# Performance work log

Measured on AMD Instinct MI355X. Metric: run time of the kernel, lower is better.

The kernel has to match this reference:

```python
import jax, jax.numpy as jnp
import numpy as np
from jax import lax

DN = ('NCHW', 'OIHW', 'NCHW')

def conv2d_s2(x, w, b):
    # nn.Conv2d(3,3,kernel=5,stride=2), VALID padding
    y = lax.conv_general_dilated(x, w, (2, 2), 'VALID', dimension_numbers=DN)
    return y + b[None, :, None, None]

def conv_transpose2d_s2_p2(x, w):
    # torch.conv_transpose2d(weight (in,out,5,5), stride=2, padding=2):
    # equivalent to conv with lhs_dilation=2, spatially flipped, IO-transposed kernel,
    # and per-side padding = k-1-p = 2.  Output H -> 2H-2.
    k = jnp.flip(w, (2, 3)).transpose(1, 0, 2, 3)
    return lax.conv_general_dilated(x, k, (1, 1), [(2, 2), (2, 2)],
                                    lhs_dilation=(2, 2), dimension_numbers=DN)

def interp_nearest(x, size):
    # F.interpolate default mode='nearest': src = floor(dst * in/out)
    H, W = x.shape[-2], x.shape[-1]
    oh, ow = size
    ri = (jnp.arange(oh) * H // oh).astype(jnp.int32)
    ci = (jnp.arange(ow) * W // ow).astype(jnp.int32)
    return x[..., ri[:, None], ci[None, :]]

def long_conv(x, conv_w, conv_b, keys, values):
    key = jax.nn.sigmoid(conv2d_s2(x, conv_w, conv_b))      # [1,3,h,w]
    key = interp_nearest(key, (32, 32)).reshape(-1)          # [3072]
    att = jax.nn.softmax(keys @ key)                         # [size]
    kernel = (values * att[:, None]).sum(0).reshape(3, 3, 5, 5)
    return conv_transpose2d_s2_p2(x, kernel)

def looper(x, conv_w, conv_b, keys, values):
    key = jax.nn.sigmoid(conv2d_s2(x, conv_w, conv_b))
    key = interp_nearest(key, (32, 32)).reshape(-1)
    att = jax.nn.softmax(keys @ key)
    return (values * att[:, None]).sum(0)                    # [1]

def setup_inputs() -> dict:
    key = jax.random.key(0)
    ks = jax.random.split(key, 8)
    cw_scale = 1.0 / np.sqrt(3 * 5 * 5)
    return {
        'input': jax.random.uniform(ks[0], (1, 3, 1024, 1024), jnp.float32),
        'lk1_conv_w': jax.random.normal(ks[1], (3, 3, 5, 5), jnp.float32) * cw_scale,
        'lk1_conv_b': jax.random.normal(ks[2], (3,), jnp.float32) * cw_scale,
        'lk1_keys': jax.random.normal(ks[3], (100, 3072), jnp.float32),
        'lk1_values': jax.random.normal(ks[4], (100, 225), jnp.float32),
        'lc_conv_w': jax.random.normal(ks[5], (3, 3, 5, 5), jnp.float32) * cw_scale,
        'lc_conv_b': jax.random.normal(ks[6], (3,), jnp.float32) * cw_scale,
        'lc_keys': jax.random.normal(ks[7], (100, 3072), jnp.float32),
        # values all 3.0 -> Looper output == 3 exactly (softmax sums to 1),
        # sigmoid(3)~0.9526 -> exactly one loop iteration, deterministically.
        'lc_values': jnp.full((100, 1), 3.0, jnp.float32),
    }

def reference(input, lk1_conv_w, lk1_conv_b, lk1_keys, lk1_values,
              lc_conv_w, lc_conv_b, lc_keys, lc_values):
    x = 2.0 * input - 1.0
    out = long_conv(x, lk1_conv_w, lk1_conv_b, lk1_keys, lk1_values)
    ix = float(jax.nn.sigmoid(looper(out, lc_conv_w, lc_conv_b, lc_keys, lc_values))[0])
    it = 0
    # data-dependent loop; exit condition evaluated eagerly (as in the torch code,
    # which syncs to host each iteration); hard cap of 10 iterations as in source.
    while ix < 1.0 and it < 10:
        it += 1
        out = long_conv(out, lk1_conv_w, lk1_conv_b, lk1_keys, lk1_values)
        ix += float(jax.nn.sigmoid(looper(out, lc_conv_w, lc_conv_b, lc_keys, lc_values))[0])
    out = jax.nn.sigmoid(out)
    return interp_nearest(out, (128, 128))
```

## Files before the change

### kernel.cpp

```cpp
#include <hip/hip_runtime.h>
#include <hip/hip_bf16.h>


#define GRID 128

#define LD1(p)     __hip_atomic_load((p), __ATOMIC_RELAXED, __HIP_MEMORY_SCOPE_AGENT)
#define ST1(p, v)  __hip_atomic_store((p), (v), __ATOMIC_RELAXED, __HIP_MEMORY_SCOPE_AGENT)

__device__ __forceinline__ float sigmoidf_(float z) {
    return 1.0f / (1.0f + expf(-z));
}

__device__ __forceinline__ void gbar(unsigned* base, int blk, int t) {
    asm volatile("s_waitcnt vmcnt(0)" ::: "memory");
    __syncthreads();
    if (t == 0) ST1(base + blk, 1u);
    if (blk == 0) {
        if (t < 128) {
            while (LD1(base + t) == 0u)
                __builtin_amdgcn_s_sleep(8);
        }
        __syncthreads();
        if (t == 0) ST1(base + 160, 1u);
    } else {
        if (t == 0) {
            while (LD1(base + 160) == 0u)
                __builtin_amdgcn_s_sleep(8);
        }
        __syncthreads();
    }
    asm volatile("" ::: "memory");
    __syncthreads();
}

__device__ __forceinline__ void key_prefetch(const float* __restrict__ in,
                                             int mul, int dbl, int blk,
                                             int lane, int wv,
                                             float xa[2], float xb[2]) {
#pragma unroll
    for (int rep = 0; rep < 2; ++rep) {
        int s = blk * 4 + wv + rep * 512;
        int ii = s >> 5, jj = s & 31;
        int qy = (ii * mul) >> 5, qx = (jj * mul) >> 5;
        int by = dbl ? 2 * qy : qy - 1;
        int bx = dbl ? 2 * qx : qx - 1;
        {
            int l = lane;
            int ci = l / 25, rm = l % 25, r = rm / 5, cc = rm % 5;
            int y = by + r, x = bx + cc;
            xa[rep] = ((unsigned)y < 1024u && (unsigned)x < 1024u)
                      ? 2.0f * in[ci * 1048576 + y * 1024 + x] - 1.0f : 0.f;
        }
        xb[rep] = 0.f;
        if (lane < 11) {
            int l = lane + 64;
            int ci = l / 25, rm = l % 25, r = rm / 5, cc = rm % 5;
            int y = by + r, x = bx + cc;
            xb[rep] = ((unsigned)y < 1024u && (unsigned)x < 1024u)
                      ? 2.0f * in[ci * 1048576 + y * 1024 + x] - 1.0f : 0.f;
        }
    }
}

__device__ __forceinline__ void key_stage(const float* __restrict__ sw,
                                          const float* __restrict__ sb,
                                          const float xa[2], const float xb[2],
                                          float* __restrict__ skv,
                                          int lane, int wv) {
#pragma unroll
    for (int rep = 0; rep < 2; ++rep) {
        float p0 = xa[rep] * sw[lane];
        float p1 = xa[rep] * sw[75 + lane];
        float p2 = xa[rep] * sw[150 + lane];
        if (lane < 11) {
            p0 += xb[rep] * sw[64 + lane];
            p1 += xb[rep] * sw[139 + lane];
            p2 += xb[rep] * sw[214 + lane];
        }
#pragma unroll
        for (int off = 32; off > 0; off >>= 1) {
            p0 += __shfl_xor(p0, off, 64);
            p1 += __shfl_xor(p1, off, 64);
            p2 += __shfl_xor(p2, off, 64);
        }
        if (lane == 0) {
            skv[0 * 8 + rep * 4 + wv] = sigmoidf_(p0 + sb[0]);
            skv[1 * 8 + rep * 4 + wv] = sigmoidf_(p1 + sb[1]);
            skv[2 * 8 + rep * 4 + wv] = sigmoidf_(p2 + sb[2]);
        }
    }
}

__device__ __forceinline__ void softmax_lds(const float* __restrict__ slog,
                                            float* __restrict__ satt,
                                            int lane, int wv) {
    if (wv == 0) {
        float v1 = slog[lane];
        float v2 = (lane + 64 < 100) ? slog[lane + 64] : -3.4e38f;
        float mx = fmaxf(v1, v2);
#pragma unroll
        for (int off = 32; off > 0; off >>= 1) mx = fmaxf(mx, __shfl_xor(mx, off, 64));
        float e1 = expf(v1 - mx);
        float e2 = (lane + 64 < 100) ? expf(v2 - mx) : 0.f;
        float s = e1 + e2;
#pragma unroll
        for (int off = 32; off > 0; off >>= 1) s += __shfl_xor(s, off, 64);
        float inv = 1.0f / s;
        satt[lane] = e1 * inv;
        if (lane + 64 < 100) satt[lane + 64] = e2 * inv;
    }
    __syncthreads();
}

__global__ __launch_bounds__(256, 1) void k_fused(
    const float* __restrict__ in, const float* __restrict__ cw,
    const float* __restrict__ cb, const float* __restrict__ keys,
    const float* __restrict__ vals, float* __restrict__ out,
    float* __restrict__ ws, unsigned* __restrict__ ctr)
{
    __shared__ float smem[11380];
    float* sk1  = smem;
    float* sk2  = smem + 232;
    float* satt = smem + 464;
    float* sw   = smem + 568;
    float* sb   = smem + 800;
    float* sW   = smem + 808;
    float* sWy  = smem + 2332;
    float* sWx  = smem + 2452;
    float* sWxy = smem + 2572;
    float* skv  = smem + 2584;
    float* slog = smem + 2608;
    float* skc  = smem + 2736;
    float* sgx  = smem + 5236;

    float* plog1 = ws;
    float* plog2 = ws + 16384;

    const int t = threadIdx.x, lane = t & 63, wv = t >> 6;
    const int blk = blockIdx.x;

    float xa1[2], xb1[2], xa2[2], xb2[2];
    key_prefetch(in, 510, 1, blk, lane, wv, xa1, xb1);
    key_prefetch(in, 1022, 0, blk, lane, wv, xa2, xb2);

    if (t < 100) {
        const float* kr = keys + t * 3072 + blk * 4;
#pragma unroll
        for (int c = 0; c < 3; ++c)
#pragma unroll
            for (int r = 0; r < 2; ++r) {
                float4 kk = *reinterpret_cast<const float4*>(kr + c * 1024 + r * 512);
                int o = t * 25 + c * 8 + r * 4;
                skc[o]     = kk.x;
                skc[o + 1] = kk.y;
                skc[o + 2] = kk.z;
                skc[o + 3] = kk.w;
            }
    }

    const int j = t & 127, h = t >> 7;
    const int R = (blk * 4093) >> 7;
    const int C = (j * 4093) >> 7;
    const int ybase = (R + 6) >> 2, r0 = (R + 6) & 3, nk = (r0 == 0) ? 4 : 3;
    const int xbase = (C + 6) >> 2, f0 = (C + 6) & 3, nl = (f0 == 0) ? 4 : 3;
#pragma unroll
    for (int k = 0; k < 4; ++k) {
        int iy = ybase - k;
#pragma unroll
        for (int lh = 0; lh < 2; ++lh) {
            int l = h * 2 + lh;
            int ix = xbase - l;
            bool ok = ((unsigned)iy < 1024u) && ((unsigned)ix < 1024u)
                      && (k < nk) && (l < nl);
            int off = iy * 1024 + ix;
            float v0 = ok ? 2.0f * in[off] - 1.0f : 0.f;
            float v1 = ok ? 2.0f * in[1048576 + off] - 1.0f : 0.f;
            float v2 = ok ? 2.0f * in[2097152 + off] - 1.0f : 0.f;
            int si = (k * 4 + l) * 128 + j;
            sgx[si]        = v0;
            sgx[2048 + si] = v1;
            sgx[4096 + si] = v2;
        }
    }

    if (t < 225) sw[t] = cw[t];
    if (t < 3)   sb[t] = cb[t];
    __syncthreads();

    key_stage(sw, sb, xa1, xb1, skv, lane, wv);
    __syncthreads();
    if (t < 100) {
        float s = 0.f;
        const float* kc = skc + t * 25;
#pragma unroll
        for (int i = 0; i < 24; ++i) s += kc[i] * skv[i];
        ST1(plog1 + blk * 128 + t, s);
    }
    gbar(ctr, blk, t);

    if (t < 100) {
        const float* p = plog1 + t;
        float s0 = 0.f, s1 = 0.f, s2 = 0.f, s3 = 0.f;
#pragma unroll
        for (int b = 0; b < 32; ++b) {
            s0 += LD1(p + (4 * b + 0) * 128);
            s1 += LD1(p + (4 * b + 1) * 128);
            s2 += LD1(p + (4 * b + 2) * 128);
            s3 += LD1(p + (4 * b + 3) * 128);
        }
        slog[t] = (s0 + s1) + (s2 + s3);
    }
    __syncthreads();
    softmax_lds(slog, satt, lane, wv);
    if (t < 225) {
        float s = 0.f;
#pragma unroll
        for (int n = 0; n < 100; ++n) s += vals[n * 225 + t] * satt[n];
        sk1[t] = s;
    }
    __syncthreads();
    if (t < 225) {
        int co = t / 75, rem = t % 75, ci = rem / 25, a = (rem % 25) / 5, bb = rem % 5;
        float s = 0.f;
#pragma unroll
        for (int c = 0; c < 5; ++c) {
            int u = c + 2 * a - 4;
            if ((unsigned)u >= 5u) continue;
#pragma unroll
            for (int d = 0; d < 5; ++d) {
                int v = d + 2 * bb - 4;
                if ((unsigned)v >= 5u) continue;
#pragma unroll
                for (int cm = 0; cm < 3; ++cm)
                    s += sk1[ci * 75 + cm * 25 + c * 5 + d] * cw[co * 75 + cm * 25 + u * 5 + v];
            }
        }
        sw[t] = s;
    }
    __syncthreads();

    key_stage(sw, sb, xa2, xb2, skv, lane, wv);
    __syncthreads();
    if (t < 100) {
        float s = 0.f;
        const float* kc = skc + t * 25;
#pragma unroll
        for (int i = 0; i < 24; ++i) s += kc[i] * skv[i];
        ST1(plog2 + blk * 128 + t, s);
    }
    gbar(ctr + 256, blk, t);

    if (t < 100) {
        const float* p = plog2 + t;
        float s0 = 0.f, s1 = 0.f, s2 = 0.f, s3 = 0.f;
#pragma unroll
        for (int b = 0; b < 32; ++b) {
            s0 += LD1(p + (4 * b + 0) * 128);
            s1 += LD1(p + (4 * b + 1) * 128);
            s2 += LD1(p + (4 * b + 2) * 128);
            s3 += LD1(p + (4 * b + 3) * 128);
        }
        slog[t] = (s0 + s1) + (s2 + s3);
    }
    __syncthreads();
    softmax_lds(slog, satt, lane, wv);
    if (t < 225) {
        float s = 0.f;
#pragma unroll
        for (int n = 0; n < 100; ++n) s += vals[n * 225 + t] * satt[n];
        sk2[t] = s;
    }
    __syncthreads();
    for (int idx = t; idx < 1521; idx += 256) {
        int ci = idx / 507, rem = idx % 507, o = rem / 169;
        int ef = rem % 169, e = ef / 13, f = ef % 13;
        float s = 0.f;
#pragma unroll
        for (int c = 0; c < 5; ++c) {
            int a = e - 2 * c;
            if ((unsigned)a >= 5u) continue;
#pragma unroll
            for (int d = 0; d < 5; ++d) {
                int b2 = f - 2 * d;
                if ((unsigned)b2 >= 5u) continue;
#pragma unroll
                for (int cm = 0; cm < 3; ++cm)
                    s += sk1[ci * 75 + cm * 25 + c * 5 + d] * sk2[cm * 75 + o * 25 + a * 5 + b2];
            }
        }
        sW[idx] = s;
    }
    if (t < 117) {
        int ci = t / 39, o = (t % 39) / 13, f = t % 13;
        float s = 0.f;
#pragma unroll
        for (int d = 0; d < 5; ++d) {
            int b2 = f - 2 * d;
            if ((unsigned)b2 >= 5u) continue;
#pragma unroll
            for (int cm = 0; cm < 3; ++cm)
                s += sk1[ci * 75 + cm * 25 + 5 + d] * sk2[cm * 75 + o * 25 + 20 + b2];
        }
        sWy[(ci * 3 + o) * 13 + f] = s;
    }
    if (t >= 128 && t < 245) {
        int q = t - 128;
        int ci = q / 39, o = (q % 39) / 13, e = q % 13;
        float s = 0.f;
#pragma unroll
        for (int c = 0; c < 5; ++c) {
            int a = e - 2 * c;
            if ((unsigned)a >= 5u) continue;
#pragma unroll
            for (int cm = 0; cm < 3; ++cm)
                s += sk1[ci * 75 + cm * 25 + c * 5 + 1] * sk2[cm * 75 + o * 25 + a * 5 + 4];
        }
        sWx[(ci * 3 + o) * 13 + e] = s;
    }
    if (t >= 246 && t < 255) {
        int q = t - 246;
        int ci = q / 3, o = q % 3;
        float s = 0.f;
#pragma unroll
        for (int cm = 0; cm < 3; ++cm)
            s += sk1[ci * 75 + cm * 25 + 5 + 1] * sk2[cm * 75 + o * 25 + 20 + 4];
        sWxy[ci * 3 + o] = s;
    }
    __syncthreads();

    if (t < 128) {
        float a0 = 0.f, a1 = 0.f, a2 = 0.f;
#pragma unroll
        for (int k = 0; k < 4; ++k) {
            if (k < nk) {
                int e = r0 + 4 * k;
#pragma unroll
                for (int l = 0; l < 4; ++l) {
                    if (l < nl) {
                        int f = f0 + 4 * l;
                        int wi = e * 13 + f;
                        int si = (k * 4 + l) * 128 + j;
                        float x0 = sgx[si], x1 = sgx[2048 + si], x2 = sgx[4096 + si];
                        a0 += x0 * sW[wi]       + x1 * sW[507 + wi]  + x2 * sW[1014 + wi];
                        a1 += x0 * sW[169 + wi] + x1 * sW[676 + wi]  + x2 * sW[1183 + wi];
                        a2 += x0 * sW[338 + wi] + x1 * sW[845 + wi]  + x2 * sW[1352 + wi];
                    }
                }
            }
        }
        if (R == 0) {
            for (int l = 0; l < nl; ++l) {
                int ix = xbase - l;
                if ((unsigned)ix >= 1024u) continue;
                int f = f0 + 4 * l;
                float x0 = 2.0f * in[ix] - 1.0f;
                float x1 = 2.0f * in[1048576 + ix] - 1.0f;
                float x2 = 2.0f * in[2097152 + ix] - 1.0f;
                a0 -= x0 * sWy[f]      + x1 * sWy[39 + f] + x2 * sWy[78 + f];
                a1 -= x0 * sWy[13 + f] + x1 * sWy[52 + f] + x2 * sWy[91 + f];
                a2 -= x0 * sWy[26 + f] + x1 * sWy[65 + f] + x2 * sWy[104 + f];
            }
        }
        if (C == 0) {
            for (int k = 0; k < nk; ++k) {
                int iy = ybase - k;
                if ((unsigned)iy >= 1024u) continue;
                int e = r0 + 4 * k;
                int off = iy * 1024;
                float x0 = 2.0f * in[off] - 1.0f;
                float x1 = 2.0f * in[1048576 + off] - 1.0f;
                float x2 = 2.0f * in[2097152 + off] - 1.0f;
                a0 -= x0 * sWx[e]      + x1 * sWx[39 + e] + x2 * sWx[78 + e];
                a1 -= x0 * sWx[13 + e] + x1 * sWx[52 + e] + x2 * sWx[91 + e];
                a2 -= x0 * sWx[26 + e] + x1 * sWx[65 + e] + x2 * sWx[104 + e];
            }
        }
        if (R == 0 && C == 0) {
            float x0 = 2.0f * in[0] - 1.0f;
            float x1 = 2.0f * in[1048576] - 1.0f;
            float x2 = 2.0f * in[2097152] - 1.0f;
            a0 += x0 * sWxy[0] + x1 * sWxy[3] + x2 * sWxy[6];
            a1 += x0 * sWxy[1] + x1 * sWxy[4] + x2 * sWxy[7];
            a2 += x0 * sWxy[2] + x1 * sWxy[5] + x2 * sWxy[8];
        }
        int T = blk * 128 + j;
        out[T]             = sigmoidf_(a0);
        out[16384 + T]     = sigmoidf_(a1);
        out[2 * 16384 + T] = sigmoidf_(a2);
    }
}

extern "C" void kernel_launch(void* const* d_in, const int* in_sizes, int n_in,
                              void* d_out, int out_size, void* d_ws, size_t ws_size,
                              hipStream_t stream) {
    const float* in   = (const float*)d_in[0];
    const float* cw   = (const float*)d_in[1];
    const float* cb   = (const float*)d_in[2];
    const float* keys = (const float*)d_in[3];
    const float* vals = (const float*)d_in[4];
    float* out = (float*)d_out;

    unsigned* ctr = (unsigned*)d_ws;
    float* wsf = (float*)((char*)d_ws + 8192);

    hipMemsetAsync(d_ws, 0, 2048, stream);
    k_fused<<<GRID, 256, 0, stream>>>(in, cw, cb, keys, vals, out, wsf, ctr);
}
```

Measured before the change: 111.2 us.

## Split logit reduction and final conv across all threads; compute only needed weight rows

Each block's cross-block logit reduction now uses two thread groups that each sum half the partial logits, and the softmax combines the two halves. The composite 13x13 kernel is now built only for the rows this block's output row actually uses, and the edge-correction weights are computed only in block 0. The final output pass is spread across both thread halves by tap column, with results combined through shared memory. The goal is to shorten the serial tail after each grid barrier, at the cost of an extra __syncthreads and more index arithmetic.

```diff
diff --git a/kernel.cpp b/kernel.cpp
--- a/kernel.cpp
+++ b/kernel.cpp
@@ -91,12 +91,32 @@
     }
 }
 
-__device__ __forceinline__ void softmax_lds(const float* __restrict__ slog,
+__device__ __forceinline__ void reduce_split(const float* __restrict__ plog,
+                                             float* __restrict__ pr0,
+                                             float* __restrict__ pr1,
+                                             int t) {
+    int g = t >> 7, tq = t & 127;
+    if (tq < 100) {
+        const float* p = plog + tq + g * 64 * 128;
+        float s0 = 0.f, s1 = 0.f, s2 = 0.f, s3 = 0.f;
+#pragma unroll
+        for (int b = 0; b < 16; ++b) {
+            s0 += LD1(p + (4 * b + 0) * 128);
+            s1 += LD1(p + (4 * b + 1) * 128);
+            s2 += LD1(p + (4 * b + 2) * 128);
+            s3 += LD1(p + (4 * b + 3) * 128);
+        }
+        (g ? pr1 : pr0)[tq] = (s0 + s1) + (s2 + s3);
+    }
+}
+
+__device__ __forceinline__ void softmax_lds(const float* __restrict__ pr0,
+                                            const float* __restrict__ pr1,
                                             float* __restrict__ satt,
                                             int lane, int wv) {
     if (wv == 0) {
-        float v1 = slog[lane];
-        float v2 = (lane + 64 < 100) ? slog[lane + 64] : -3.4e38f;
+        float v1 = pr0[lane] + pr1[lane];
+        float v2 = (lane + 64 < 100) ? pr0[lane + 64] + pr1[lane + 64] : -3.4e38f;
         float mx = fmaxf(v1, v2);
 #pragma unroll
         for (int off = 32; off > 0; off >>= 1) mx = fmaxf(mx, __shfl_xor(mx, off, 64));
@@ -118,20 +138,22 @@
     const float* __restrict__ vals, float* __restrict__ out,
     float* __restrict__ ws, unsigned* __restrict__ ctr)
 {
-    __shared__ float smem[11380];
+    __shared__ float smem[10704];
     float* sk1  = smem;
     float* sk2  = smem + 232;
     float* satt = smem + 464;
     float* sw   = smem + 568;
     float* sb   = smem + 800;
-    float* sW   = smem + 808;
-    float* sWy  = smem + 2332;
-    float* sWx  = smem + 2452;
-    float* sWxy = smem + 2572;
-    float* skv  = smem + 2584;
-    float* slog = smem + 2608;
-    float* skc  = smem + 2736;
-    float* sgx  = smem + 5236;
+    float* skv  = smem + 808;
+    float* pr0  = smem + 832;
+    float* pr1  = smem + 936;
+    float* skc  = smem + 1040;
+    float* sWk  = smem + 3540;
+    float* sWxk = smem + 4008;
+    float* sWy  = smem + 4044;
+    float* sWxy = smem + 4164;
+    float* sga  = smem + 4176;
+    float* sgx  = smem + 4560;
 
     float* plog1 = ws;
     float* plog2 = ws + 16384;
@@ -163,6 +185,7 @@
     const int C = (j * 4093) >> 7;
     const int ybase = (R + 6) >> 2, r0 = (R + 6) & 3, nk = (r0 == 0) ? 4 : 3;
     const int xbase = (C + 6) >> 2, f0 = (C + 6) & 3, nl = (f0 == 0) ? 4 : 3;
+    const int nk13 = nk * 13;
 #pragma unroll
     for (int k = 0; k < 4; ++k) {
         int iy = ybase - k;
@@ -198,25 +221,17 @@
     }
     gbar(ctr, blk, t);
 
-    if (t < 100) {
-        const float* p = plog1 + t;
-        float s0 = 0.f, s1 = 0.f, s2 = 0.f, s3 = 0.f;
-#pragma unroll
-        for (int b = 0; b < 32; ++b) {
-            s0 += LD1(p + (4 * b + 0) * 128);
-            s1 += LD1(p + (4 * b + 1) * 128);
-            s2 += LD1(p + (4 * b + 2) * 128);
-            s3 += LD1(p + (4 * b + 3) * 128);
-        }
-        slog[t] = (s0 + s1) + (s2 + s3);
-    }
-    __syncthreads();
-    softmax_lds(slog, satt, lane, wv);
+    reduce_split(plog1, pr0, pr1, t);
+    __syncthreads();
+    softmax_lds(pr0, pr1, satt, lane, wv);
     if (t < 225) {
-        float s = 0.f;
-#pragma unroll
-        for (int n = 0; n < 100; ++n) s += vals[n * 225 + t] * satt[n];
-        sk1[t] = s;
+        float sa = 0.f, sb2 = 0.f;
+#pragma unroll
+        for (int n = 0; n < 50; ++n) {
+            sa  += vals[(2 * n) * 225 + t] * satt[2 * n];
+            sb2 += vals[(2 * n + 1) * 225 + t] * satt[2 * n + 1];
+        }
+        sk1[t] = sa + sb2;
     }
     __syncthreads();
     if (t < 225) {
@@ -250,30 +265,24 @@
     }
     gbar(ctr + 256, blk, t);
 
-    if (t < 100) {
-        const float* p = plog2 + t;
-        float s0 = 0.f, s1 = 0.f, s2 = 0.f, s3 = 0.f;
-#pragma unroll
-        for (int b = 0; b < 32; ++b) {
-            s0 += LD1(p + (4 * b + 0) * 128);
-            s1 += LD1(p + (4 * b + 1) * 128);
-            s2 += LD1(p + (4 * b + 2) * 128);
-            s3 += LD1(p + (4 * b + 3) * 128);
-        }
-        slog[t] = (s0 + s1) + (s2 + s3);
-    }
-    __syncthreads();
-    softmax_lds(slog, satt, lane, wv);
+    reduce_split(plog2, pr0, pr1, t);
+    __syncthreads();
+    softmax_lds(pr0, pr1, satt, lane, wv);
     if (t < 225) {
-        float s = 0.f;
-#pragma unroll
-        for (int n = 0; n < 100; ++n) s += vals[n * 225 + t] * satt[n];
-        sk2[t] = s;
-    }
-    __syncthreads();
-    for (int idx = t; idx < 1521; idx += 256) {
-        int ci = idx / 507, rem = idx % 507, o = rem / 169;
-        int ef = rem % 169, e = ef / 13, f = ef % 13;
+        float sa = 0.f, sb2 = 0.f;
+#pragma unroll
+        for (int n = 0; n < 50; ++n) {
+            sa  += vals[(2 * n) * 225 + t] * satt[2 * n];
+            sb2 += vals[(2 * n + 1) * 225 + t] * satt[2 * n + 1];
+        }
+        sk2[t] = sa + sb2;
+    }
+    __syncthreads();
+    for (int idx = t; idx < 9 * nk13; idx += 256) {
+        int cio = idx / nk13, rem = idx % nk13;
+        int k = rem / 13, f = rem % 13;
+        int e = r0 + 4 * k;
+        int ci = cio / 3, o = cio % 3;
         float s = 0.f;
 #pragma unroll
         for (int c = 0; c < 5; ++c) {
@@ -288,24 +297,13 @@
                     s += sk1[ci * 75 + cm * 25 + c * 5 + d] * sk2[cm * 75 + o * 25 + a * 5 + b2];
             }
         }
-        sW[idx] = s;
-    }
-    if (t < 117) {
-        int ci = t / 39, o = (t % 39) / 13, f = t % 13;
-        float s = 0.f;
-#pragma unroll
-        for (int d = 0; d < 5; ++d) {
-            int b2 = f - 2 * d;
-            if ((unsigned)b2 >= 5u) continue;
-#pragma unroll
-            for (int cm = 0; cm < 3; ++cm)
-                s += sk1[ci * 75 + cm * 25 + 5 + d] * sk2[cm * 75 + o * 25 + 20 + b2];
-        }
-        sWy[(ci * 3 + o) * 13 + f] = s;
-    }
-    if (t >= 128 && t < 245) {
+        sWk[idx] = s;
+    }
+    if (t >= 128 && t < 128 + 9 * nk) {
         int q = t - 128;
-        int ci = q / 39, o = (q % 39) / 13, e = q % 13;
+        int cio = q / nk, k = q % nk;
+        int e = r0 + 4 * k;
+        int ci = cio / 3, o = cio % 3;
         float s = 0.f;
 #pragma unroll
         for (int c = 0; c < 5; ++c) {
@@ -315,67 +313,90 @@
             for (int cm = 0; cm < 3; ++cm)
                 s += sk1[ci * 75 + cm * 25 + c * 5 + 1] * sk2[cm * 75 + o * 25 + a * 5 + 4];
         }
-        sWx[(ci * 3 + o) * 13 + e] = s;
-    }
-    if (t >= 246 && t < 255) {
-        int q = t - 246;
-        int ci = q / 3, o = q % 3;
-        float s = 0.f;
-#pragma unroll
-        for (int cm = 0; cm < 3; ++cm)
-            s += sk1[ci * 75 + cm * 25 + 5 + 1] * sk2[cm * 75 + o * 25 + 20 + 4];
-        sWxy[ci * 3 + o] = s;
-    }
-    __syncthreads();
-
-    if (t < 128) {
+        sWxk[cio * nk + k] = s;
+    }
+    if (blk == 0) {
+        if (t < 117) {
+            int ci = t / 39, o = (t % 39) / 13, f = t % 13;
+            float s = 0.f;
+#pragma unroll
+            for (int d = 0; d < 5; ++d) {
+                int b2 = f - 2 * d;
+                if ((unsigned)b2 >= 5u) continue;
+#pragma unroll
+                for (int cm = 0; cm < 3; ++cm)
+                    s += sk1[ci * 75 + cm * 25 + 5 + d] * sk2[cm * 75 + o * 25 + 20 + b2];
+            }
+            sWy[(ci * 3 + o) * 13 + f] = s;
+        }
+        if (t >= 224 && t < 233) {
+            int q = t - 224;
+            int ci = q / 3, o = q % 3;
+            float s = 0.f;
+#pragma unroll
+            for (int cm = 0; cm < 3; ++cm)
+                s += sk1[ci * 75 + cm * 25 + 5 + 1] * sk2[cm * 75 + o * 25 + 20 + 4];
+            sWxy[ci * 3 + o] = s;
+        }
+    }
+    __syncthreads();
+
+    {
         float a0 = 0.f, a1 = 0.f, a2 = 0.f;
 #pragma unroll
         for (int k = 0; k < 4; ++k) {
             if (k < nk) {
-                int e = r0 + 4 * k;
-#pragma unroll
-                for (int l = 0; l < 4; ++l) {
+#pragma unroll
+                for (int lh = 0; lh < 2; ++lh) {
+                    int l = h * 2 + lh;
                     if (l < nl) {
                         int f = f0 + 4 * l;
-                        int wi = e * 13 + f;
+                        int wi = k * 13 + f;
                         int si = (k * 4 + l) * 128 + j;
                         float x0 = sgx[si], x1 = sgx[2048 + si], x2 = sgx[4096 + si];
-                        a0 += x0 * sW[wi]       + x1 * sW[507 + wi]  + x2 * sW[1014 + wi];
-                        a1 += x0 * sW[169 + wi] + x1 * sW[676 + wi]  + x2 * sW[1183 + wi];
-                        a2 += x0 * sW[338 + wi] + x1 * sW[845 + wi]  + x2 * sW[1352 + wi];
+                        a0 += x0 * sWk[wi]            + x1 * sWk[3 * nk13 + wi] + x2 * sWk[6 * nk13 + wi];
+                        a1 += x0 * sWk[nk13 + wi]     + x1 * sWk[4 * nk13 + wi] + x2 * sWk[7 * nk13 + wi];
+                        a2 += x0 * sWk[2 * nk13 + wi] + x1 * sWk[5 * nk13 + wi] + x2 * sWk[8 * nk13 + wi];
                     }
                 }
             }
         }
         if (R == 0) {
-            for (int l = 0; l < nl; ++l) {
-                int ix = xbase - l;
-                if ((unsigned)ix >= 1024u) continue;
-                int f = f0 + 4 * l;
-                float x0 = 2.0f * in[ix] - 1.0f;
-                float x1 = 2.0f * in[1048576 + ix] - 1.0f;
-                float x2 = 2.0f * in[2097152 + ix] - 1.0f;
-                a0 -= x0 * sWy[f]      + x1 * sWy[39 + f] + x2 * sWy[78 + f];
-                a1 -= x0 * sWy[13 + f] + x1 * sWy[52 + f] + x2 * sWy[91 + f];
-                a2 -= x0 * sWy[26 + f] + x1 * sWy[65 + f] + x2 * sWy[104 + f];
-            }
-        }
-        if (C == 0) {
-            for (int k = 0; k < nk; ++k) {
-                int iy = ybase - k;
-                if ((unsigned)iy >= 1024u) continue;
-                int e = r0 + 4 * k;
-                int off = iy * 1024;
-                float x0 = 2.0f * in[off] - 1.0f;
-                float x1 = 2.0f * in[1048576 + off] - 1.0f;
-                float x2 = 2.0f * in[2097152 + off] - 1.0f;
-                a0 -= x0 * sWx[e]      + x1 * sWx[39 + e] + x2 * sWx[78 + e];
-                a1 -= x0 * sWx[13 + e] + x1 * sWx[52 + e] + x2 * sWx[91 + e];
-                a2 -= x0 * sWx[26 + e] + x1 * sWx[65 + e] + x2 * sWx[104 + e];
-            }
-        }
-        if (R == 0 && C == 0) {
+#pragma unroll
+            for (int lh = 0; lh < 2; ++lh) {
+                int l = h * 2 + lh;
+                if (l < nl) {
+                    int ix = xbase - l;
+                    if ((unsigned)ix < 1024u) {
+                        int f = f0 + 4 * l;
+                        float x0 = 2.0f * in[ix] - 1.0f;
+                        float x1 = 2.0f * in[1048576 + ix] - 1.0f;
+                        float x2 = 2.0f * in[2097152 + ix] - 1.0f;
+                        a0 -= x0 * sWy[f]      + x1 * sWy[39 + f] + x2 * sWy[78 + f];
+                        a1 -= x0 * sWy[13 + f] + x1 * sWy[52 + f] + x2 * sWy[91 + f];
+                        a2 -= x0 * sWy[26 + f] + x1 * sWy[65 + f] + x2 * sWy[104 + f];
+                    }
+                }
+            }
+        }
+        if (C == 0 && h == 0) {
+#pragma unroll
+            for (int k = 0; k < 4; ++k) {
+                if (k < nk) {
+                    int iy = ybase - k;
+                    if ((unsigned)iy < 1024u) {
+                        int off = iy * 1024;
+                        float x0 = 2.0f * in[off] - 1.0f;
+                        float x1 = 2.0f * in[1048576 + off] - 1.0f;
+                        float x2 = 2.0f * in[2097152 + off] - 1.0f;
+                        a0 -= x0 * sWxk[k]          + x1 * sWxk[3 * nk + k] + x2 * sWxk[6 * nk + k];
+                        a1 -= x0 * sWxk[nk + k]     + x1 * sWxk[4 * nk + k] + x2 * sWxk[7 * nk + k];
+                        a2 -= x0 * sWxk[2 * nk + k] + x1 * sWxk[5 * nk + k] + x2 * sWxk[8 * nk + k];
+                    }
+                }
+            }
+        }
+        if (R == 0 && C == 0 && h == 0) {
             float x0 = 2.0f * in[0] - 1.0f;
             float x1 = 2.0f * in[1048576] - 1.0f;
             float x2 = 2.0f * in[2097152] - 1.0f;
@@ -383,10 +404,16 @@
             a1 += x0 * sWxy[1] + x1 * sWxy[4] + x2 * sWxy[7];
             a2 += x0 * sWxy[2] + x1 * sWxy[5] + x2 * sWxy[8];
         }
-        int T = blk * 128 + j;
-        out[T]             = sigmoidf_(a0);
-        out[16384 + T]     = sigmoidf_(a1);
-        out[2 * 16384 + T] = sigmoidf_(a2);
+        if (h == 1) {
+            sga[j] = a0; sga[128 + j] = a1; sga[256 + j] = a2;
+        }
+        __syncthreads();
+        if (h == 0) {
+            int T = blk * 128 + j;
+            out[T]             = sigmoidf_(a0 + sga[j]);
+            out[16384 + T]     = sigmoidf_(a1 + sga[128 + j]);
+            out[2 * 16384 + T] = sigmoidf_(a2 + sga[256 + j]);
+        }
     }
 }
 
```

Result: faster. 107.6 us (-3.2%).
